# Kernel tuning notes

Hardware: AMD Instinct MI355X
Metric: run time of the kernel (lower is better)

The kernel has to match this reference:

```python
import jax, jax.numpy as jnp
import numpy as np
import math

C = 256
K = 64
STAGE_NUM = 3
UNFOLD_SIZES = (1, 3, 5)


def _l2norm(t, axis):
    return t / (1e-6 + jnp.linalg.norm(t, axis=axis, keepdims=True))


def setup_inputs() -> dict:
    key = jax.random.key(0)
    k0, k1, k2 = jax.random.split(key, 3)
    b, h, w = 4, 64, 64
    x = jax.random.normal(k0, (b, C, h, w), dtype=jnp.float32)
    mu0 = jax.random.normal(k1, (1, C, K), dtype=jnp.float32) * math.sqrt(2.0 / K)
    mu0 = _l2norm(mu0, axis=1)  # matches buffer init: normal_(0, sqrt(2/k)) then l2norm over c
    w_scalar = jnp.array(1.0, dtype=jnp.float32)
    # convcat: Conv2d(3c, c, 1); init std = sqrt(2 / (1*1*out_channels)) = sqrt(2/c)
    w_cat = jax.random.normal(k2, (C, 3 * C), dtype=jnp.float32) * math.sqrt(2.0 / C)
    b_cat = jnp.zeros((C,), dtype=jnp.float32)
    return {"x": x, "mu0": mu0, "w": w_scalar, "w_cat": w_cat, "b_cat": b_cat}


def _mwi_forward(x, mu0, w, w_cat, b_cat):
    b, c, h, wd = x.shape
    k = mu0.shape[2]
    mu = jnp.broadcast_to(mu0, (b, c, k))
    feats = []
    for s in UNFOLD_SIZES:
        p = (s - 1) // 2
        xp = jnp.pad(x, ((0, 0), (0, 0), (p, p), (p, p)))
        # im2col: (b, c, s*s, h, w), kernel positions row-major -> matches torch F.unfold then view(b,c,-1)
        patches = jnp.stack([xp[:, :, i:i + h, j:j + wd] for i in range(s) for j in range(s)], axis=2)
        ux = patches.reshape(b, c, s * s * h * wd)  # (b, c, N)
        z = None
        for _ in range(STAGE_NUM):  # EM iterations (no_grad in original)
            z = jax.nn.softmax(jnp.einsum('bcn,bck->bnk', ux, mu), axis=2)  # E-step
            z_ = z / (1e-6 + z.sum(axis=1, keepdims=True))
            mu = _l2norm(jnp.einsum('bcn,bnk->bck', ux, z_), axis=1)  # M-step
        mu = jax.lax.stop_gradient(mu)
        z = jax.lax.stop_gradient(z)
        zf = jnp.einsum('bck,bnk->bcn', mu, z)  # reconstruction (b, c, N)
        zf = zf.reshape(b, c, s, s, h, wd)
        # col2im (F.fold): overlap-add of kernel positions
        out = jnp.zeros((b, c, h + 2 * p, wd + 2 * p), dtype=x.dtype)
        for i in range(s):
            for j in range(s):
                out = out.at[:, :, i:i + h, j:j + wd].add(zf[:, :, i, j])
        feats.append(out[:, :, p:p + h, p:p + wd])
    cat = jnp.concatenate(feats, axis=1)  # (b, 3c, h, w)
    u = jnp.einsum('bihw,oi->bohw', cat, w_cat) + b_cat[None, :, None, None]
    out = jax.nn.relu(u * w + x)
    return out, mu


def reference(x, mu0, w, w_cat, b_cat):
    return _mwi_forward(x, mu0, w, w_cat, b_cat)
```

## Files before the change

### kernel.cpp

```cpp
#include <hip/hip_runtime.h>

typedef float f32x4 __attribute__((ext_vector_type(4)));
typedef short bf16x8 __attribute__((ext_vector_type(8)));
typedef unsigned short u16;
typedef u16 u16x8 __attribute__((ext_vector_type(8)));
typedef unsigned int u32;

#define B 4
#define C 256
#define K 64
#define NN 4096
#define W3C 768
#define CP 264
#define SP 72
#define LGP 68

__device__ __forceinline__ u16 bf_hi(float f) {
    unsigned u = __float_as_uint(f);
    u += 0x7FFFu + ((u >> 16) & 1u);
    return (u16)(u >> 16);
}
__device__ __forceinline__ float bf_f(u16 s) { return __uint_as_float(((unsigned)s) << 16); }

__global__ void k_prep(const float* __restrict__ x, const float* __restrict__ mu0,
                       const float* __restrict__ w_cat,
                       u16* __restrict__ xch, u16* __restrict__ xcl,
                       u16* __restrict__ wch, u16* __restrict__ wcl,
                       u16* __restrict__ muth, u16* __restrict__ mutl,
                       u16* __restrict__ xth, u16* __restrict__ xtl) {
    __shared__ float tile[32][33];
    int blk = blockIdx.x, tid = threadIdx.x;
    if (blk < 2048) {
        int i = blk * 256 + tid;
        const float4* s4 = (const float4*)(x + (size_t)i * 8);
        float4 a = s4[0], bq = s4[1];
        float v[8] = {a.x, a.y, a.z, a.w, bq.x, bq.y, bq.z, bq.w};
        u16x8 hv, lv;
        #pragma unroll
        for (int j = 0; j < 8; j++) { u16 hh = bf_hi(v[j]); hv[j] = hh; lv[j] = bf_hi(v[j] - bf_f(hh)); }
        *(u16x8*)(xch + (size_t)i * 8) = hv;
        *(u16x8*)(xcl + (size_t)i * 8) = lv;
    } else if (blk < 2144) {
        int i = (blk - 2048) * 256 + tid;
        const float4* s4 = (const float4*)(w_cat + (size_t)i * 8);
        float4 a = s4[0], bq = s4[1];
        float v[8] = {a.x, a.y, a.z, a.w, bq.x, bq.y, bq.z, bq.w};
        u16x8 hv, lv;
        #pragma unroll
        for (int j = 0; j < 8; j++) { u16 hh = bf_hi(v[j]); hv[j] = hh; lv[j] = bf_hi(v[j] - bf_f(hh)); }
        *(u16x8*)(wch + (size_t)i * 8) = hv;
        *(u16x8*)(wcl + (size_t)i * 8) = lv;
    } else if (blk < 2400) {
        int g = (blk - 2144) * 256 + tid;
        int kq = (g >> 8) & 63, cq = g & 255;
        float v = mu0[cq * K + kq];
        u16 hh = bf_hi(v);
        muth[g] = hh;
        mutl[g] = bf_hi(v - bf_f(hh));
    } else {
        int t = blk - 2400;
        int b2 = t >> 10, rem = t & 1023;
        int c0 = (rem >> 7) << 5, m0 = (rem & 127) << 5;
        int tx = tid & 31, ty = tid >> 5;
        #pragma unroll
        for (int j = 0; j < 4; j++)
            tile[ty + j * 8][tx] = x[((size_t)(b2 * C + c0 + ty + j * 8)) * NN + m0 + tx];
        __syncthreads();
        #pragma unroll
        for (int j = 0; j < 4; j++) {
            int n = m0 + ty + j * 8;
            float v = tile[tx][ty + j * 8];
            u16 hh = bf_hi(v);
            size_t o = ((size_t)(b2 * NN + n)) * C + c0 + tx;
            xth[o] = hh;
            xtl[o] = bf_hi(v - bf_f(hh));
        }
    }
}

__global__ __launch_bounds__(512) void k_em(
        const u16* __restrict__ xth, const u16* __restrict__ xtl,
        const u16* __restrict__ xch, const u16* __restrict__ xcl,
        const u16* __restrict__ muth, const u16* __restrict__ mutl,
        float* __restrict__ tpart, float* __restrict__ dpart,
        u16* __restrict__ sig_out, int pv, int write_sig)
{
    extern __shared__ char smem[];
    u16* smh = (u16*)smem;
    u16* sml = smh + 64 * CP;
    float* slog = (float*)(sml + 64 * CP);
    u16* sTh = (u16*)(slog + 64 * LGP);
    u16* sTl = sTh + 64 * SP;
    float* redf = (float*)(sTl + 64 * SP);

    const int ch = blockIdx.x, b = blockIdx.y, tid = threadIdx.x;
    const int n0 = ch * 64;
    const int w = tid >> 6, l = tid & 63, lg = l >> 4, lr = l & 15;
    const int chalf = (w >> 2) * 128;
    f32x4 z4 = {0.f, 0.f, 0.f, 0.f};

    {
        size_t mbase = (size_t)(b * K) * C;
        #pragma unroll
        for (int t = tid; t < 2048; t += 512) {
            int r = t >> 5, cof = (t & 31) * 8;
            *(u16x8*)&smh[r * CP + cof] = *(const u16x8*)&muth[mbase + (size_t)r * C + cof];
            *(u16x8*)&sml[r * CP + cof] = *(const u16x8*)&mutl[mbase + (size_t)r * C + cof];
        }
    }
    bf16x8 eAh[4], eAl[4];
    {
        const u16* xrh = xth + ((size_t)(b * NN + n0 + (w & 3) * 16 + lr)) * C + chalf;
        const u16* xrl = xtl + ((size_t)(b * NN + n0 + (w & 3) * 16 + lr)) * C + chalf;
        #pragma unroll
        for (int cc = 0; cc < 4; cc++) {
            eAh[cc] = *(const bf16x8*)&xrh[cc * 32 + lg * 8];
            eAl[cc] = *(const bf16x8*)&xrl[cc * 32 + lg * 8];
        }
    }
    bf16x8 mBh[4], mBl[4];
    #pragma unroll
    for (int nn2 = 0; nn2 < 2; nn2++)
        #pragma unroll
        for (int cio = 0; cio < 2; cio++) {
            int c = (w * 2 + cio) * 16 + lr;
            size_t go = ((size_t)(b * C + c)) * NN + n0 + nn2 * 32 + lg * 8;
            mBh[nn2 * 2 + cio] = *(const bf16x8*)&xch[go];
            mBl[nn2 * 2 + cio] = *(const bf16x8*)&xcl[go];
        }
    __syncthreads();

    f32x4 acc[4] = {z4, z4, z4, z4};
    #pragma unroll
    for (int cc = 0; cc < 4; cc++) {
        int co = chalf + cc * 32 + lg * 8;
        #pragma unroll
        for (int kt = 0; kt < 4; kt++) {
            bf16x8 Bh = *(bf16x8*)&smh[(kt * 16 + lr) * CP + co];
            bf16x8 Bl = *(bf16x8*)&sml[(kt * 16 + lr) * CP + co];
            acc[kt] = __builtin_amdgcn_mfma_f32_16x16x32_bf16(eAh[cc], Bh, acc[kt], 0, 0, 0);
            acc[kt] = __builtin_amdgcn_mfma_f32_16x16x32_bf16(eAl[cc], Bh, acc[kt], 0, 0, 0);
            acc[kt] = __builtin_amdgcn_mfma_f32_16x16x32_bf16(eAh[cc], Bl, acc[kt], 0, 0, 0);
        }
    }
    if (w < 4) {
        #pragma unroll
        for (int kt = 0; kt < 4; kt++)
            #pragma unroll
            for (int jj = 0; jj < 4; jj++)
                slog[((w & 3) * 16 + lg * 4 + jj) * LGP + kt * 16 + lr] = acc[kt][jj];
    }
    __syncthreads();

    if (w >= 4) {
        float swv[4][4];
        float psum[4] = {0.f, 0.f, 0.f, 0.f};
        #pragma unroll
        for (int jj = 0; jj < 4; jj++) {
            int rloc = (w & 3) * 16 + lg * 4 + jj;
            int n = n0 + rloc;
            float v0 = acc[0][jj] + slog[rloc * LGP + 0 * 16 + lr];
            float v1 = acc[1][jj] + slog[rloc * LGP + 1 * 16 + lr];
            float v2 = acc[2][jj] + slog[rloc * LGP + 2 * 16 + lr];
            float v3 = acc[3][jj] + slog[rloc * LGP + 3 * 16 + lr];
            float m = fmaxf(fmaxf(v0, v1), fmaxf(v2, v3));
            #pragma unroll
            for (int off = 1; off <= 8; off <<= 1) m = fmaxf(m, __shfl_xor(m, off));
            float e0 = __expf(v0 - m), e1 = __expf(v1 - m), e2 = __expf(v2 - m), e3 = __expf(v3 - m);
            float ss = e0 + e1 + e2 + e3;
            #pragma unroll
            for (int off = 1; off <= 8; off <<= 1) ss += __shfl_xor(ss, off);
            int y = n >> 6, xx = n & 63;
            float cntw = (float)((min(pv, y) + min(pv, 63 - y) + 1) * (min(pv, xx) + min(pv, 63 - xx) + 1));
            float sc = cntw / ss;
            swv[jj][0] = e0 * sc; swv[jj][1] = e1 * sc; swv[jj][2] = e2 * sc; swv[jj][3] = e3 * sc;
            #pragma unroll
            for (int kt = 0; kt < 4; kt++) {
                psum[kt] += swv[jj][kt];
                if (write_sig)
                    sig_out[((size_t)(b * NN + n)) * K + kt * 16 + lr] = bf_hi(swv[jj][kt]);
            }
        }
        #pragma unroll
        for (int kt = 0; kt < 4; kt++) {
            #pragma unroll
            for (int jp = 0; jp < 2; jp++) {
                float va = swv[2 * jp][kt], vb = swv[2 * jp + 1][kt];
                u16 ha = bf_hi(va), hb = bf_hi(vb);
                u16 la = bf_hi(va - bf_f(ha)), lb = bf_hi(vb - bf_f(hb));
                int col = (w & 3) * 16 + lg * 4 + 2 * jp;
                *(u32*)&sTh[(kt * 16 + lr) * SP + col] = (u32)ha | ((u32)hb << 16);
                *(u32*)&sTl[(kt * 16 + lr) * SP + col] = (u32)la | ((u32)lb << 16);
            }
            redf[(kt * 16 + lr) * 17 + (w & 3) * 4 + lg] = psum[kt];
        }
    }
    __syncthreads();
    if (tid < 64) {
        float sd = 0.f;
        #pragma unroll
        for (int g2 = 0; g2 < 16; g2++) sd += redf[tid * 17 + g2];
        dpart[((size_t)(b * 64 + ch)) * K + tid] = sd;
    }

    f32x4 macc[8];
    #pragma unroll
    for (int t2 = 0; t2 < 8; t2++) macc[t2] = z4;
    #pragma unroll
    for (int nn2 = 0; nn2 < 2; nn2++) {
        int no = nn2 * 32 + lg * 8;
        bf16x8 Ah[4], Al[4];
        #pragma unroll
        for (int kt2 = 0; kt2 < 4; kt2++) {
            Ah[kt2] = *(bf16x8*)&sTh[(kt2 * 16 + lr) * SP + no];
            Al[kt2] = *(bf16x8*)&sTl[(kt2 * 16 + lr) * SP + no];
        }
        #pragma unroll
        for (int cio = 0; cio < 2; cio++) {
            #pragma unroll
            for (int kt2 = 0; kt2 < 4; kt2++) {
                macc[kt2 * 2 + cio] = __builtin_amdgcn_mfma_f32_16x16x32_bf16(Ah[kt2], mBh[nn2 * 2 + cio], macc[kt2 * 2 + cio], 0, 0, 0);
                macc[kt2 * 2 + cio] = __builtin_amdgcn_mfma_f32_16x16x32_bf16(Al[kt2], mBh[nn2 * 2 + cio], macc[kt2 * 2 + cio], 0, 0, 0);
                macc[kt2 * 2 + cio] = __builtin_amdgcn_mfma_f32_16x16x32_bf16(Ah[kt2], mBl[nn2 * 2 + cio], macc[kt2 * 2 + cio], 0, 0, 0);
            }
        }
    }
    #pragma unroll
    for (int kt2 = 0; kt2 < 4; kt2++)
        #pragma unroll
        for (int cio = 0; cio < 2; cio++)
            #pragma unroll
            for (int jj = 0; jj < 4; jj++) {
                int kk = kt2 * 16 + lg * 4 + jj;
                int c = (w * 2 + cio) * 16 + lr;
                tpart[((size_t)((b * 64 + ch) * K + kk)) * C + c] = macc[kt2 * 2 + cio][jj];
            }
}

__global__ __launch_bounds__(256) void k_norm(
        const float* __restrict__ tpart, const float* __restrict__ dpart,
        u16* __restrict__ muth, u16* __restrict__ mutl,
        u16* __restrict__ Pb, const u16* __restrict__ wch, const u16* __restrict__ wcl,
        float* __restrict__ out_mu, float dconst, int s_pm, int last) {
    __shared__ float red[256];
    __shared__ float murow[256];
    __shared__ float dsh;
    int k = blockIdx.x, b = blockIdx.y, tid = threadIdx.x;
    float dv = 0.f;
    if (tid < 64) dv = dpart[((size_t)(b * 64 + tid)) * K + k];
    #pragma unroll
    for (int off = 1; off <= 32; off <<= 1) dv += __shfl_xor(dv, off);
    if (tid == 0) dsh = dv;
    float tt = 0.f;
    #pragma unroll 8
    for (int chn = 0; chn < 64; chn++)
        tt += tpart[((size_t)((b * 64 + chn) * K + k)) * C + tid];
    red[tid] = tt * tt;
    __syncthreads();
    for (int st = 128; st > 0; st >>= 1) {
        if (tid < st) red[tid] += red[tid + st];
        __syncthreads();
    }
    float d = dconst + dsh;
    float inv = 1.f / (1e-6f * d + sqrtf(red[0]));
    float v = tt * inv;
    murow[tid] = v;
    u16 hh = bf_hi(v);
    size_t o = ((size_t)(b * K + k)) * C + tid;
    muth[o] = hh;
    mutl[o] = bf_hi(v - bf_f(hh));
    if (last) out_mu[((size_t)(b * C + tid)) * K + k] = v;
    if (s_pm >= 0) {
        __syncthreads();
        const u16* wh = wch + (size_t)tid * W3C + s_pm * C;
        const u16* wl = wcl + (size_t)tid * W3C + s_pm * C;
        float accp = 0.f;
        #pragma unroll 4
        for (int c8 = 0; c8 < 32; c8++) {
            u16x8 hv = *(const u16x8*)&wh[c8 * 8];
            u16x8 lv = *(const u16x8*)&wl[c8 * 8];
            #pragma unroll
            for (int j = 0; j < 8; j++)
                accp += (bf_f(hv[j]) + bf_f(lv[j])) * murow[c8 * 8 + j];
        }
        Pb[((size_t)((s_pm * B + b) * C + tid)) * K + k] = bf_hi(accp);
    }
}

__global__ __launch_bounds__(256) void k_final(
        const u16* __restrict__ sh_g, const u16* __restrict__ Pb,
        const float* __restrict__ x, const float* __restrict__ b_cat,
        const float* __restrict__ wscal, float* __restrict__ out) {
    __shared__ u16 ssig[64 * 72];
    __shared__ u16 sP[64 * 72];
    __shared__ float tbuf[64 * 68];
    int nt = blockIdx.x, ot = blockIdx.y, b = blockIdx.z;
    int n0 = nt * 64, o0 = ot * 64;
    int tid = threadIdx.x, w = tid >> 6, l = tid & 63, lg = l >> 4, lr = l & 15;
    f32x4 z4 = {0.f, 0.f, 0.f, 0.f};
    f32x4 acc[4] = {z4, z4, z4, z4};
    for (int s = 0; s < 3; s++) {
        __syncthreads();
        for (int t = tid; t < 512; t += 256) {
            int r = t >> 3, kc = (t & 7) * 8;
            *(u16x8*)&ssig[r * 72 + kc] =
                *(const u16x8*)&sh_g[(size_t)s * ((size_t)B * NN * K) + ((size_t)(b * NN + n0 + r)) * K + kc];
            *(u16x8*)&sP[r * 72 + kc] =
                *(const u16x8*)&Pb[((size_t)((s * B + b) * C + o0 + r)) * K + kc];
        }
        __syncthreads();
        #pragma unroll
        for (int kk = 0; kk < 2; kk++) {
            int ko = kk * 32 + lg * 8;
            bf16x8 A = *(bf16x8*)&ssig[(w * 16 + lr) * 72 + ko];
            #pragma unroll
            for (int oi = 0; oi < 4; oi++) {
                bf16x8 Bv = *(bf16x8*)&sP[(oi * 16 + lr) * 72 + ko];
                acc[oi] = __builtin_amdgcn_mfma_f32_16x16x32_bf16(A, Bv, acc[oi], 0, 0, 0);
            }
        }
    }
    __syncthreads();
    #pragma unroll
    for (int oi = 0; oi < 4; oi++)
        #pragma unroll
        for (int jj = 0; jj < 4; jj++)
            tbuf[(oi * 16 + lr) * 68 + (w * 16 + lg * 4 + jj)] = acc[oi][jj];
    __syncthreads();
    float wv = wscal[0];
    for (int t = tid; t < 1024; t += 256) {
        int ol = t >> 4, ck = (t & 15) * 4;
        int o = o0 + ol;
        float bc = b_cat[o];
        float4 u4 = *(float4*)&tbuf[ol * 68 + ck];
        size_t base = ((size_t)(b * C + o)) * NN + n0 + ck;
        float4 xv = *(const float4*)&x[base];
        float4 r;
        r.x = fmaxf((u4.x + bc) * wv + xv.x, 0.f);
        r.y = fmaxf((u4.y + bc) * wv + xv.y, 0.f);
        r.z = fmaxf((u4.z + bc) * wv + xv.z, 0.f);
        r.w = fmaxf((u4.w + bc) * wv + xv.w, 0.f);
        *(float4*)&out[base] = r;
    }
}

extern "C" void kernel_launch(void* const* d_in, const int* in_sizes, int n_in,
                              void* d_out, int out_size, void* d_ws, size_t ws_size,
                              hipStream_t stream) {
    const float* x     = (const float*)d_in[0];
    const float* mu0   = (const float*)d_in[1];
    const float* wsc   = (const float*)d_in[2];
    const float* w_cat = (const float*)d_in[3];
    const float* b_cat = (const float*)d_in[4];
    float* out = (float*)d_out;
    char* wsb = (char*)d_ws;

    const size_t SZ_X2   = (size_t)B * C * NN * 2;
    const size_t SZ_MUT  = (size_t)B * K * C * 2;
    const size_t SZ_SIGH = (size_t)3 * B * NN * K * 2;
    const size_t SZ_TP   = (size_t)B * 64 * K * C * 4;
    const size_t SZ_DP   = (size_t)B * 64 * K * 4;
    const size_t SZ_PB   = (size_t)3 * B * C * K * 2;
    const size_t SZ_WC   = (size_t)C * W3C * 2;

    size_t off = 0;
    u16*   xch  = (u16*)(wsb + off); off += SZ_X2;
    u16*   xcl  = (u16*)(wsb + off); off += SZ_X2;
    u16*   xth  = (u16*)(wsb + off); off += SZ_X2;
    u16*   xtl  = (u16*)(wsb + off); off += SZ_X2;
    u16*   muth = (u16*)(wsb + off); off += SZ_MUT;
    u16*   mutl = (u16*)(wsb + off); off += SZ_MUT;
    u16*   sigh = (u16*)(wsb + off); off += SZ_SIGH;
    float* tpart= (float*)(wsb + off); off += SZ_TP;
    float* dpart= (float*)(wsb + off); off += SZ_DP;
    u16*   Pb   = (u16*)(wsb + off); off += SZ_PB;
    u16*   wch  = (u16*)(wsb + off); off += SZ_WC;
    u16*   wcl  = (u16*)(wsb + off); off += SZ_WC;
    float* out_mu = out + (size_t)B * C * NN;

    const int EM_LDS = 2 * 64 * CP * 2 + 64 * LGP * 4 + 2 * 64 * SP * 2 + 1152 * 4;
    hipFuncSetAttribute((const void*)k_em, hipFuncAttributeMaxDynamicSharedMemorySize, EM_LDS);

    k_prep<<<6496, 256, 0, stream>>>(x, mu0, w_cat, xch, xcl, wch, wcl, muth, mutl, xth, xtl);

    const float dconsts[3] = {1e-6f, 1e-6f + 11.9375f, 1e-6f + 59.4375f};

    for (int i = 0; i < 9; i++) {
        int s = i / 3;
        u16* shs = sigh + (size_t)s * ((size_t)B * NN * K);
        k_em<<<dim3(64, B), 512, EM_LDS, stream>>>(
            xth, xtl, xch, xcl, muth, mutl, tpart, dpart, shs, s, (i % 3 == 2) ? 1 : 0);
        k_norm<<<dim3(K, B), 256, 0, stream>>>(
            tpart, dpart, muth, mutl, Pb, wch, wcl, out_mu,
            dconsts[s], (i % 3 == 2) ? s : -1, (i == 8) ? 1 : 0);
    }
    k_final<<<dim3(64, 4, B), 256, 0, stream>>>(sigh, Pb, x, b_cat, wsc, out);
}
```

Measured before the change: 259.6 us.

## Fuse mu normalization into EM kernel via per-batch atomic grid barrier

The separate k_norm launch after each of the nine EM steps is removed. Its reduction, normalization, mu write-back and W_cat projection now run at the end of k_em, after a per-batch spin barrier on an atomic counter. The counters are zeroed in k_prep. The prep kernel is also restructured so that each transpose tile writes both the channel-major and the transposed bf16 hi/lo copies of x, so x is read once instead of twice. This is meant to cut kernel launch and drain overhead and prep traffic. It relies on all 64 blocks per batch being co-resident, otherwise the spin barrier could deadlock.

```diff
diff --git a/kernel.cpp b/kernel.cpp
--- a/kernel.cpp
+++ b/kernel.cpp
@@ -25,23 +25,35 @@
 __global__ void k_prep(const float* __restrict__ x, const float* __restrict__ mu0,
                        const float* __restrict__ w_cat,
                        u16* __restrict__ xch, u16* __restrict__ xcl,
+                       u16* __restrict__ xth, u16* __restrict__ xtl,
                        u16* __restrict__ wch, u16* __restrict__ wcl,
                        u16* __restrict__ muth, u16* __restrict__ mutl,
-                       u16* __restrict__ xth, u16* __restrict__ xtl) {
+                       u32* __restrict__ cnt) {
     __shared__ float tile[32][33];
     int blk = blockIdx.x, tid = threadIdx.x;
-    if (blk < 2048) {
-        int i = blk * 256 + tid;
-        const float4* s4 = (const float4*)(x + (size_t)i * 8);
-        float4 a = s4[0], bq = s4[1];
-        float v[8] = {a.x, a.y, a.z, a.w, bq.x, bq.y, bq.z, bq.w};
-        u16x8 hv, lv;
-        #pragma unroll
-        for (int j = 0; j < 8; j++) { u16 hh = bf_hi(v[j]); hv[j] = hh; lv[j] = bf_hi(v[j] - bf_f(hh)); }
-        *(u16x8*)(xch + (size_t)i * 8) = hv;
-        *(u16x8*)(xcl + (size_t)i * 8) = lv;
-    } else if (blk < 2144) {
-        int i = (blk - 2048) * 256 + tid;
+    if (blk < 4096) {
+        int b2 = blk >> 10, rem = blk & 1023;
+        int c0 = (rem >> 7) << 5, m0 = (rem & 127) << 5;
+        int tx = tid & 31, ty = tid >> 5;
+        #pragma unroll
+        for (int j = 0; j < 4; j++)
+            tile[ty + j * 8][tx] = x[((size_t)(b2 * C + c0 + ty + j * 8)) * NN + m0 + tx];
+        __syncthreads();
+        #pragma unroll
+        for (int j = 0; j < 4; j++) {
+            float vc = tile[ty + j * 8][tx];
+            u16 hc = bf_hi(vc);
+            size_t oc = ((size_t)(b2 * C + c0 + ty + j * 8)) * NN + m0 + tx;
+            xch[oc] = hc;
+            xcl[oc] = bf_hi(vc - bf_f(hc));
+            float vt = tile[tx][ty + j * 8];
+            u16 ht = bf_hi(vt);
+            size_t ot = ((size_t)(b2 * NN + m0 + ty + j * 8)) * C + c0 + tx;
+            xth[ot] = ht;
+            xtl[ot] = bf_hi(vt - bf_f(ht));
+        }
+    } else if (blk < 4192) {
+        int i = (blk - 4096) * 256 + tid;
         const float4* s4 = (const float4*)(w_cat + (size_t)i * 8);
         float4 a = s4[0], bq = s4[1];
         float v[8] = {a.x, a.y, a.z, a.w, bq.x, bq.y, bq.z, bq.w};
@@ -50,40 +62,27 @@
         for (int j = 0; j < 8; j++) { u16 hh = bf_hi(v[j]); hv[j] = hh; lv[j] = bf_hi(v[j] - bf_f(hh)); }
         *(u16x8*)(wch + (size_t)i * 8) = hv;
         *(u16x8*)(wcl + (size_t)i * 8) = lv;
-    } else if (blk < 2400) {
-        int g = (blk - 2144) * 256 + tid;
+    } else if (blk < 4448) {
+        int g = (blk - 4192) * 256 + tid;
         int kq = (g >> 8) & 63, cq = g & 255;
         float v = mu0[cq * K + kq];
         u16 hh = bf_hi(v);
         muth[g] = hh;
         mutl[g] = bf_hi(v - bf_f(hh));
     } else {
-        int t = blk - 2400;
-        int b2 = t >> 10, rem = t & 1023;
-        int c0 = (rem >> 7) << 5, m0 = (rem & 127) << 5;
-        int tx = tid & 31, ty = tid >> 5;
-        #pragma unroll
-        for (int j = 0; j < 4; j++)
-            tile[ty + j * 8][tx] = x[((size_t)(b2 * C + c0 + ty + j * 8)) * NN + m0 + tx];
-        __syncthreads();
-        #pragma unroll
-        for (int j = 0; j < 4; j++) {
-            int n = m0 + ty + j * 8;
-            float v = tile[tx][ty + j * 8];
-            u16 hh = bf_hi(v);
-            size_t o = ((size_t)(b2 * NN + n)) * C + c0 + tx;
-            xth[o] = hh;
-            xtl[o] = bf_hi(v - bf_f(hh));
-        }
+        if (tid < 40) cnt[tid] = 0;
     }
 }
 
 __global__ __launch_bounds__(512) void k_em(
         const u16* __restrict__ xth, const u16* __restrict__ xtl,
         const u16* __restrict__ xch, const u16* __restrict__ xcl,
-        const u16* __restrict__ muth, const u16* __restrict__ mutl,
+        u16* __restrict__ muth, u16* __restrict__ mutl,
         float* __restrict__ tpart, float* __restrict__ dpart,
-        u16* __restrict__ sig_out, int pv, int write_sig)
+        u16* __restrict__ sig_out, u16* __restrict__ Pb,
+        const u16* __restrict__ wch, const u16* __restrict__ wcl,
+        float* __restrict__ out_mu, u32* __restrict__ cnt,
+        int iter, int pv, float dconst, int write_sig, int s_pm, int last)
 {
     extern __shared__ char smem[];
     u16* smh = (u16*)smem;
@@ -235,55 +234,73 @@
                 int c = (w * 2 + cio) * 16 + lr;
                 tpart[((size_t)((b * 64 + ch) * K + kk)) * C + c] = macc[kt2 * 2 + cio][jj];
             }
-}
-
-__global__ __launch_bounds__(256) void k_norm(
-        const float* __restrict__ tpart, const float* __restrict__ dpart,
-        u16* __restrict__ muth, u16* __restrict__ mutl,
-        u16* __restrict__ Pb, const u16* __restrict__ wch, const u16* __restrict__ wcl,
-        float* __restrict__ out_mu, float dconst, int s_pm, int last) {
-    __shared__ float red[256];
-    __shared__ float murow[256];
-    __shared__ float dsh;
-    int k = blockIdx.x, b = blockIdx.y, tid = threadIdx.x;
+
+    __syncthreads();
+    if (tid == 0) {
+        __threadfence();
+        __hip_atomic_fetch_add(&cnt[iter * B + b], 1u, __ATOMIC_ACQ_REL, __HIP_MEMORY_SCOPE_AGENT);
+        while (__hip_atomic_load(&cnt[iter * B + b], __ATOMIC_ACQUIRE, __HIP_MEMORY_SCOPE_AGENT) < 64u)
+            __builtin_amdgcn_s_sleep(2);
+        __threadfence();
+    }
+    __syncthreads();
+
+    int cc2 = tid & 255, h2 = tid >> 8;
+    float tt = 0.f;
+    #pragma unroll 4
+    for (int chn = 0; chn < 32; chn++)
+        tt += tpart[((size_t)((b * 64 + h2 * 32 + chn) * K + ch)) * C + cc2];
+    redf[tid] = tt;
     float dv = 0.f;
-    if (tid < 64) dv = dpart[((size_t)(b * 64 + tid)) * K + k];
-    #pragma unroll
-    for (int off = 1; off <= 32; off <<= 1) dv += __shfl_xor(dv, off);
-    if (tid == 0) dsh = dv;
-    float tt = 0.f;
-    #pragma unroll 8
-    for (int chn = 0; chn < 64; chn++)
-        tt += tpart[((size_t)((b * 64 + chn) * K + k)) * C + tid];
-    red[tid] = tt * tt;
-    __syncthreads();
-    for (int st = 128; st > 0; st >>= 1) {
-        if (tid < st) red[tid] += red[tid + st];
-        __syncthreads();
-    }
-    float d = dconst + dsh;
-    float inv = 1.f / (1e-6f * d + sqrtf(red[0]));
-    float v = tt * inv;
-    murow[tid] = v;
-    u16 hh = bf_hi(v);
-    size_t o = ((size_t)(b * K + k)) * C + tid;
-    muth[o] = hh;
-    mutl[o] = bf_hi(v - bf_f(hh));
-    if (last) out_mu[((size_t)(b * C + tid)) * K + k] = v;
+    if (tid < 64) {
+        dv = dpart[((size_t)(b * 64 + tid)) * K + ch];
+        #pragma unroll
+        for (int off = 1; off <= 32; off <<= 1) dv += __shfl_xor(dv, off);
+    }
+    __syncthreads();
+    float ttf = 0.f;
+    if (h2 == 0) {
+        ttf = redf[cc2] + redf[cc2 + 256];
+        redf[512 + cc2] = ttf * ttf;
+    }
+    if (tid == 0) redf[1024] = dv;
+    __syncthreads();
+    if (tid < 64) {
+        float sq = redf[512 + tid] + redf[512 + tid + 64] + redf[512 + tid + 128] + redf[512 + tid + 192];
+        #pragma unroll
+        for (int off = 1; off <= 32; off <<= 1) sq += __shfl_xor(sq, off);
+        if (tid == 0) redf[1025] = sq;
+    }
+    __syncthreads();
+    float d = dconst + redf[1024];
+    float inv = 1.f / (1e-6f * d + sqrtf(redf[1025]));
+    if (h2 == 0) {
+        float v = ttf * inv;
+        u16 hh = bf_hi(v);
+        size_t o = ((size_t)(b * K + ch)) * C + cc2;
+        muth[o] = hh;
+        mutl[o] = bf_hi(v - bf_f(hh));
+        if (last) out_mu[((size_t)(b * C + cc2)) * K + ch] = v;
+        slog[cc2] = v;
+    }
+    __syncthreads();
+
     if (s_pm >= 0) {
-        __syncthreads();
-        const u16* wh = wch + (size_t)tid * W3C + s_pm * C;
-        const u16* wl = wcl + (size_t)tid * W3C + s_pm * C;
+        const u16* wh = wch + (size_t)cc2 * W3C + s_pm * C + h2 * 128;
+        const u16* wl = wcl + (size_t)cc2 * W3C + s_pm * C + h2 * 128;
         float accp = 0.f;
         #pragma unroll 4
-        for (int c8 = 0; c8 < 32; c8++) {
+        for (int c8 = 0; c8 < 16; c8++) {
             u16x8 hv = *(const u16x8*)&wh[c8 * 8];
             u16x8 lv = *(const u16x8*)&wl[c8 * 8];
             #pragma unroll
             for (int j = 0; j < 8; j++)
-                accp += (bf_f(hv[j]) + bf_f(lv[j])) * murow[c8 * 8 + j];
-        }
-        Pb[((size_t)((s_pm * B + b) * C + tid)) * K + k] = bf_hi(accp);
+                accp += (bf_f(hv[j]) + bf_f(lv[j])) * slog[h2 * 128 + c8 * 8 + j];
+        }
+        redf[tid] = accp;
+        __syncthreads();
+        if (h2 == 0)
+            Pb[((size_t)((s_pm * B + b) * C + cc2)) * K + ch] = bf_hi(redf[cc2] + redf[cc2 + 256]);
     }
 }
 
@@ -376,12 +393,14 @@
     u16*   Pb   = (u16*)(wsb + off); off += SZ_PB;
     u16*   wch  = (u16*)(wsb + off); off += SZ_WC;
     u16*   wcl  = (u16*)(wsb + off); off += SZ_WC;
+    u32*   cnt  = (u32*)(wsb + off); off += 256;
     float* out_mu = out + (size_t)B * C * NN;
 
     const int EM_LDS = 2 * 64 * CP * 2 + 64 * LGP * 4 + 2 * 64 * SP * 2 + 1152 * 4;
     hipFuncSetAttribute((const void*)k_em, hipFuncAttributeMaxDynamicSharedMemorySize, EM_LDS);
 
-    k_prep<<<6496, 256, 0, stream>>>(x, mu0, w_cat, xch, xcl, wch, wcl, muth, mutl, xth, xtl);
+    k_prep<<<4449, 256, 0, stream>>>(x, mu0, w_cat, xch, xcl, xth, xtl,
+                                     wch, wcl, muth, mutl, cnt);
 
     const float dconsts[3] = {1e-6f, 1e-6f + 11.9375f, 1e-6f + 59.4375f};
 
@@ -389,10 +408,10 @@
         int s = i / 3;
         u16* shs = sigh + (size_t)s * ((size_t)B * NN * K);
         k_em<<<dim3(64, B), 512, EM_LDS, stream>>>(
-            xth, xtl, xch, xcl, muth, mutl, tpart, dpart, shs, s, (i % 3 == 2) ? 1 : 0);
-        k_norm<<<dim3(K, B), 256, 0, stream>>>(
-            tpart, dpart, muth, mutl, Pb, wch, wcl, out_mu,
-            dconsts[s], (i % 3 == 2) ? s : -1, (i == 8) ? 1 : 0);
+            xth, xtl, xch, xcl, muth, mutl, tpart, dpart, shs, Pb, wch, wcl,
+            out_mu, cnt,
+            i, s, dconsts[s], (i % 3 == 2) ? 1 : 0, (i % 3 == 2) ? s : -1,
+            (i == 8) ? 1 : 0);
     }
     k_final<<<dim3(64, 4, B), 256, 0, stream>>>(sigh, Pb, x, b_cat, wsc, out);
 }
```

New measurement: 545.0 us. +109.9%, slower.

## Fuse x bf16 split passes and read mu fragments directly from global

Applied to the files above, without the earlier changes.

The prep kernel now produces both the channel-major and the transposed hi/lo bf16 copies of x from a single shared-memory tile, so x is read from global memory once instead of twice. The EM kernel no longer stages the mu hi/lo matrices into shared memory before the E-step. Each wave loads its MFMA B fragments straight from global memory, which drops one barrier and about 67 KB of LDS per block and may allow more blocks per CU. The cost is redundant global or L2 reads of mu across the eight waves, plus load latency inside the MFMA loop.

```diff
diff --git a/kernel.cpp b/kernel.cpp
--- a/kernel.cpp
+++ b/kernel.cpp
@@ -11,7 +11,6 @@
 #define K 64
 #define NN 4096
 #define W3C 768
-#define CP 264
 #define SP 72
 #define LGP 68
 
@@ -25,23 +24,34 @@
 __global__ void k_prep(const float* __restrict__ x, const float* __restrict__ mu0,
                        const float* __restrict__ w_cat,
                        u16* __restrict__ xch, u16* __restrict__ xcl,
+                       u16* __restrict__ xth, u16* __restrict__ xtl,
                        u16* __restrict__ wch, u16* __restrict__ wcl,
-                       u16* __restrict__ muth, u16* __restrict__ mutl,
-                       u16* __restrict__ xth, u16* __restrict__ xtl) {
+                       u16* __restrict__ muth, u16* __restrict__ mutl) {
     __shared__ float tile[32][33];
     int blk = blockIdx.x, tid = threadIdx.x;
-    if (blk < 2048) {
-        int i = blk * 256 + tid;
-        const float4* s4 = (const float4*)(x + (size_t)i * 8);
-        float4 a = s4[0], bq = s4[1];
-        float v[8] = {a.x, a.y, a.z, a.w, bq.x, bq.y, bq.z, bq.w};
-        u16x8 hv, lv;
-        #pragma unroll
-        for (int j = 0; j < 8; j++) { u16 hh = bf_hi(v[j]); hv[j] = hh; lv[j] = bf_hi(v[j] - bf_f(hh)); }
-        *(u16x8*)(xch + (size_t)i * 8) = hv;
-        *(u16x8*)(xcl + (size_t)i * 8) = lv;
-    } else if (blk < 2144) {
-        int i = (blk - 2048) * 256 + tid;
+    if (blk < 4096) {
+        int b2 = blk >> 10, rem = blk & 1023;
+        int c0 = (rem >> 7) << 5, m0 = (rem & 127) << 5;
+        int tx = tid & 31, ty = tid >> 5;
+        #pragma unroll
+        for (int j = 0; j < 4; j++)
+            tile[ty + j * 8][tx] = x[((size_t)(b2 * C + c0 + ty + j * 8)) * NN + m0 + tx];
+        __syncthreads();
+        #pragma unroll
+        for (int j = 0; j < 4; j++) {
+            float vc = tile[ty + j * 8][tx];
+            u16 hc = bf_hi(vc);
+            size_t oc = ((size_t)(b2 * C + c0 + ty + j * 8)) * NN + m0 + tx;
+            xch[oc] = hc;
+            xcl[oc] = bf_hi(vc - bf_f(hc));
+            float vt = tile[tx][ty + j * 8];
+            u16 ht = bf_hi(vt);
+            size_t ot = ((size_t)(b2 * NN + m0 + ty + j * 8)) * C + c0 + tx;
+            xth[ot] = ht;
+            xtl[ot] = bf_hi(vt - bf_f(ht));
+        }
+    } else if (blk < 4192) {
+        int i = (blk - 4096) * 256 + tid;
         const float4* s4 = (const float4*)(w_cat + (size_t)i * 8);
         float4 a = s4[0], bq = s4[1];
         float v[8] = {a.x, a.y, a.z, a.w, bq.x, bq.y, bq.z, bq.w};
@@ -50,31 +60,13 @@
         for (int j = 0; j < 8; j++) { u16 hh = bf_hi(v[j]); hv[j] = hh; lv[j] = bf_hi(v[j] - bf_f(hh)); }
         *(u16x8*)(wch + (size_t)i * 8) = hv;
         *(u16x8*)(wcl + (size_t)i * 8) = lv;
-    } else if (blk < 2400) {
-        int g = (blk - 2144) * 256 + tid;
+    } else {
+        int g = (blk - 4192) * 256 + tid;
         int kq = (g >> 8) & 63, cq = g & 255;
         float v = mu0[cq * K + kq];
         u16 hh = bf_hi(v);
         muth[g] = hh;
         mutl[g] = bf_hi(v - bf_f(hh));
-    } else {
-        int t = blk - 2400;
-        int b2 = t >> 10, rem = t & 1023;
-        int c0 = (rem >> 7) << 5, m0 = (rem & 127) << 5;
-        int tx = tid & 31, ty = tid >> 5;
-        #pragma unroll
-        for (int j = 0; j < 4; j++)
-            tile[ty + j * 8][tx] = x[((size_t)(b2 * C + c0 + ty + j * 8)) * NN + m0 + tx];
-        __syncthreads();
-        #pragma unroll
-        for (int j = 0; j < 4; j++) {
-            int n = m0 + ty + j * 8;
-            float v = tile[tx][ty + j * 8];
-            u16 hh = bf_hi(v);
-            size_t o = ((size_t)(b2 * NN + n)) * C + c0 + tx;
-            xth[o] = hh;
-            xtl[o] = bf_hi(v - bf_f(hh));
-        }
     }
 }
 
@@ -86,9 +78,7 @@
         u16* __restrict__ sig_out, int pv, int write_sig)
 {
     extern __shared__ char smem[];
-    u16* smh = (u16*)smem;
-    u16* sml = smh + 64 * CP;
-    float* slog = (float*)(sml + 64 * CP);
+    float* slog = (float*)smem;
     u16* sTh = (u16*)(slog + 64 * LGP);
     u16* sTl = sTh + 64 * SP;
     float* redf = (float*)(sTl + 64 * SP);
@@ -99,15 +89,6 @@
     const int chalf = (w >> 2) * 128;
     f32x4 z4 = {0.f, 0.f, 0.f, 0.f};
 
-    {
-        size_t mbase = (size_t)(b * K) * C;
-        #pragma unroll
-        for (int t = tid; t < 2048; t += 512) {
-            int r = t >> 5, cof = (t & 31) * 8;
-            *(u16x8*)&smh[r * CP + cof] = *(const u16x8*)&muth[mbase + (size_t)r * C + cof];
-            *(u16x8*)&sml[r * CP + cof] = *(const u16x8*)&mutl[mbase + (size_t)r * C + cof];
-        }
-    }
     bf16x8 eAh[4], eAl[4];
     {
         const u16* xrh = xth + ((size_t)(b * NN + n0 + (w & 3) * 16 + lr)) * C + chalf;
@@ -128,19 +109,22 @@
             mBh[nn2 * 2 + cio] = *(const bf16x8*)&xch[go];
             mBl[nn2 * 2 + cio] = *(const bf16x8*)&xcl[go];
         }
-    __syncthreads();
 
     f32x4 acc[4] = {z4, z4, z4, z4};
-    #pragma unroll
-    for (int cc = 0; cc < 4; cc++) {
-        int co = chalf + cc * 32 + lg * 8;
-        #pragma unroll
-        for (int kt = 0; kt < 4; kt++) {
-            bf16x8 Bh = *(bf16x8*)&smh[(kt * 16 + lr) * CP + co];
-            bf16x8 Bl = *(bf16x8*)&sml[(kt * 16 + lr) * CP + co];
-            acc[kt] = __builtin_amdgcn_mfma_f32_16x16x32_bf16(eAh[cc], Bh, acc[kt], 0, 0, 0);
-            acc[kt] = __builtin_amdgcn_mfma_f32_16x16x32_bf16(eAl[cc], Bh, acc[kt], 0, 0, 0);
-            acc[kt] = __builtin_amdgcn_mfma_f32_16x16x32_bf16(eAh[cc], Bl, acc[kt], 0, 0, 0);
+    {
+        const u16* mrh = muth + ((size_t)(b * K + lr)) * C + chalf;
+        const u16* mrl = mutl + ((size_t)(b * K + lr)) * C + chalf;
+        #pragma unroll
+        for (int cc = 0; cc < 4; cc++) {
+            int co = cc * 32 + lg * 8;
+            #pragma unroll
+            for (int kt = 0; kt < 4; kt++) {
+                bf16x8 Bh = *(const bf16x8*)&mrh[(size_t)(kt * 16) * C + co];
+                bf16x8 Bl = *(const bf16x8*)&mrl[(size_t)(kt * 16) * C + co];
+                acc[kt] = __builtin_amdgcn_mfma_f32_16x16x32_bf16(eAh[cc], Bh, acc[kt], 0, 0, 0);
+                acc[kt] = __builtin_amdgcn_mfma_f32_16x16x32_bf16(eAl[cc], Bh, acc[kt], 0, 0, 0);
+                acc[kt] = __builtin_amdgcn_mfma_f32_16x16x32_bf16(eAh[cc], Bl, acc[kt], 0, 0, 0);
+            }
         }
     }
     if (w < 4) {
@@ -378,10 +362,11 @@
     u16*   wcl  = (u16*)(wsb + off); off += SZ_WC;
     float* out_mu = out + (size_t)B * C * NN;
 
-    const int EM_LDS = 2 * 64 * CP * 2 + 64 * LGP * 4 + 2 * 64 * SP * 2 + 1152 * 4;
+    const int EM_LDS = 64 * LGP * 4 + 2 * 64 * SP * 2 + 1152 * 4;
     hipFuncSetAttribute((const void*)k_em, hipFuncAttributeMaxDynamicSharedMemorySize, EM_LDS);
 
-    k_prep<<<6496, 256, 0, stream>>>(x, mu0, w_cat, xch, xcl, wch, wcl, muth, mutl, xth, xtl);
+    k_prep<<<4448, 256, 0, stream>>>(x, mu0, w_cat, xch, xcl, xth, xtl,
+                                     wch, wcl, muth, mutl);
 
     const float dconsts[3] = {1e-6f, 1e-6f + 11.9375f, 1e-6f + 59.4375f};
 
```

After: 298.1 us. 1.15x slower.
